# Kernel optimization log

Measured on AMD Instinct MI355X. Metric: run time of the kernel, lower is better.

Reference implementation:

```python
import jax, jax.numpy as jnp
import numpy as np

MARGIN = 0.2
EPS = 1e-8
N, D_EMB, N_CLASSES = 8192, 256, 512


def setup_inputs() -> dict:
    key = jax.random.key(0)
    k1, k2 = jax.random.split(key)
    embeddings = jax.random.normal(k1, (N, D_EMB), dtype=jnp.float32)
    labels = jax.random.randint(k2, (N,), 0, N_CLASSES, dtype=jnp.int64)
    return {"embeddings": embeddings, "labels": labels}


def reference(embeddings, labels):
    # OnlineTripleLoss.forward with sampling_strategy='fixed_semi_hard', cosine metric.
    n = embeddings.shape[0]
    norms = jnp.linalg.norm(embeddings, axis=1, keepdims=True)
    xn = embeddings / jnp.maximum(norms, EPS)
    dist = 1.0 - xn @ xn.T                       # [N, N] cosine distance

    same = labels[:, None] == labels[None, :]    # same-label mask
    neg_mask = ~same
    has_neg = jnp.any(neg_mask, axis=1)          # anchor has at least one negative

    # fixed_semi_hard argmax(ap+margin-an) == argmin(an); fallback is also argmin(an)
    BIG = jnp.float32(1e9)
    dmin_neg = jnp.min(jnp.where(neg_mask, dist, BIG), axis=1)  # [N]

    # all anchor-positive combinations: same label, a < p (itertools.combinations order)
    upper = jnp.triu(jnp.ones((n, n), dtype=bool), 1)
    pair_mask = same & upper & has_neg[:, None]

    losses = jnp.maximum(dist - dmin_neg[:, None] + MARGIN, 0.0)
    count = jnp.sum(pair_mask)
    loss_sum = jnp.sum(jnp.where(pair_mask, losses, 0.0))
    loss = jnp.where(count > 0, loss_sum / jnp.maximum(count, 1).astype(jnp.float32), 0.0)
    return loss, count
```

## Files before the change

kernel.cpp:

```cpp
#include <hip/hip_runtime.h>
#include <hip/hip_bf16.h>

#define NROWS 8192
#define DEMB 256
#define MARGIN 0.2f
#define BM 128
#define BK 64
#define NT (NROWS / BM)
#define NBLK (NT * (NT + 1) / 2)
#define NCLS 512
#define NCAP 96

typedef __attribute__((ext_vector_type(4))) float f32x4;
typedef __attribute__((ext_vector_type(8))) short bf16x8;

static __device__ __forceinline__ unsigned short f2b(float f) {
    unsigned u = __builtin_bit_cast(unsigned, f);
    u += 0x7fffu + ((u >> 16) & 1u);
    return (unsigned short)(u >> 16);
}
static __device__ __forceinline__ float b2f(unsigned short b) {
    unsigned u = ((unsigned)b) << 16;
    return __builtin_bit_cast(float, u);
}
static __device__ __forceinline__ unsigned encf(float f) {
    unsigned u = __builtin_bit_cast(unsigned, f);
    return (u & 0x80000000u) ? ~u : (u | 0x80000000u);
}
static __device__ __forceinline__ float decf(unsigned e) {
    unsigned u = (e & 0x80000000u) ? (e ^ 0x80000000u) : ~e;
    return __builtin_bit_cast(float, u);
}
static __device__ __forceinline__ void gload16(const void* g, void* l) {
    __builtin_amdgcn_global_load_lds(
        (const __attribute__((address_space(1))) unsigned int*)g,
        (__attribute__((address_space(3))) unsigned int*)l, 16, 0, 0);
}

__global__ __launch_bounds__(256) void k_norm(const float* __restrict__ x,
                                              unsigned short* __restrict__ xnb) {
    int row  = (blockIdx.x * blockDim.x + threadIdx.x) >> 6;
    int lane = threadIdx.x & 63;
    const float4* p = reinterpret_cast<const float4*>(x + (size_t)row * DEMB) + lane;
    float4 v = *p;
    float s = v.x * v.x + v.y * v.y + v.z * v.z + v.w * v.w;
#pragma unroll
    for (int m = 1; m < 64; m <<= 1) s += __shfl_xor(s, m);
    float inv = 1.0f / fmaxf(sqrtf(s), 1e-8f);
    ushort4 o;
    o.x = f2b(v.x * inv); o.y = f2b(v.y * inv);
    o.z = f2b(v.z * inv); o.w = f2b(v.w * inv);
    *(reinterpret_cast<ushort4*>(xnb + (size_t)row * DEMB) + lane) = o;
}

__global__ __launch_bounds__(256, 2) void k_maxneg(const unsigned short* __restrict__ xnb,
                                                   const int* __restrict__ labels,
                                                   unsigned* __restrict__ amax) {
    extern __shared__ char lds[];
    unsigned short* tile = (unsigned short*)lds;
    __shared__ int slabR[128], slabC[128];

    int tid  = threadIdx.x;
    int wid  = tid >> 6, lane = tid & 63;
    int wr   = wid >> 1, wc = wid & 1;
    int arow = lane & 15, kgrp = lane >> 4;
    int sw   = (arow & 7) << 4;

    int bi = 0, rem = blockIdx.x;
    while (rem >= NT - bi) { rem -= NT - bi; ++bi; }
    int bj = bi + rem;
    int i0 = bi * BM;
    int j0 = bj * BM;

    if (tid < 128)      slabR[tid]       = labels[i0 + tid];
    else                slabC[tid - 128] = labels[j0 + tid - 128];

    const unsigned short* Ag = xnb + (size_t)i0 * DEMB;
    const unsigned short* Bg = xnb + (size_t)j0 * DEMB;

    int c0 = (kgrp * 16) ^ sw;
    int c1 = (64 + kgrp * 16) ^ sw;
    int abase = (wr * 64 + arow) * 128;
    int bbase = (wc * 64 + arow) * 128;

    f32x4 acc[4][4] = {};

    auto stage = [&](int buf, int k0) {
#pragma unroll
        for (int i = 0; i < 4; ++i) {
            int idx  = i * 256 + tid;
            int row  = idx >> 3;
            int colb = (idx & 7) << 4;
            int scol = (colb ^ ((row & 7) << 4)) >> 1;
            const unsigned short* sa = Ag + (size_t)row * DEMB + k0 + scol;
            const unsigned short* sb = Bg + (size_t)row * DEMB + k0 + scol;
            unsigned short* da = tile + buf * 8192 + i * 2048 + wid * 512;
            unsigned short* db = tile + 16384 + buf * 8192 + i * 2048 + wid * 512;
            gload16(sa, da);
            gload16(sb, db);
        }
    };

    stage(0, 0);
#pragma unroll
    for (int ks = 0; ks < 4; ++ks) {
        __syncthreads();
        if (ks < 3) stage((ks + 1) & 1, (ks + 1) * BK);
        const char* At = (const char*)(tile + (ks & 1) * 8192);
        const char* Bt = (const char*)(tile + 16384 + (ks & 1) * 8192);
        bf16x8 a[4][2], b[4][2];
#pragma unroll
        for (int m = 0; m < 4; ++m) {
            a[m][0] = *(const bf16x8*)(At + abase + m * 2048 + c0);
            a[m][1] = *(const bf16x8*)(At + abase + m * 2048 + c1);
            b[m][0] = *(const bf16x8*)(Bt + bbase + m * 2048 + c0);
            b[m][1] = *(const bf16x8*)(Bt + bbase + m * 2048 + c1);
        }
#pragma unroll
        for (int m = 0; m < 4; ++m)
#pragma unroll
            for (int n = 0; n < 4; ++n) {
                acc[m][n] = __builtin_amdgcn_mfma_f32_16x16x32_bf16(a[m][0], b[n][0], acc[m][n], 0, 0, 0);
                acc[m][n] = __builtin_amdgcn_mfma_f32_16x16x32_bf16(a[m][1], b[n][1], acc[m][n], 0, 0, 0);
            }
    }

    __syncthreads();
    float* smaxr = (float*)tile;
    float* smaxc = (float*)tile + 256;

    int cl[4];
#pragma unroll
    for (int n = 0; n < 4; ++n) cl[n] = slabC[wc * 64 + n * 16 + arow];

    float cmx[4] = {-1e30f, -1e30f, -1e30f, -1e30f};
#pragma unroll
    for (int m = 0; m < 4; ++m) {
#pragma unroll
        for (int r = 0; r < 4; ++r) {
            int rl = slabR[wr * 64 + m * 16 + kgrp * 4 + r];
            float v = -1e30f;
#pragma unroll
            for (int n = 0; n < 4; ++n) {
                float av = acc[m][n][r];
                if (cl[n] != rl) {
                    v = fmaxf(v, av);
                    cmx[n] = fmaxf(cmx[n], av);
                }
            }
#pragma unroll
            for (int msk = 1; msk < 16; msk <<= 1) v = fmaxf(v, __shfl_xor(v, msk));
            if (arow == 0) smaxr[wc * 128 + wr * 64 + m * 16 + kgrp * 4 + r] = v;
        }
    }
#pragma unroll
    for (int n = 0; n < 4; ++n) {
        float w = cmx[n];
        w = fmaxf(w, __shfl_xor(w, 16));
        w = fmaxf(w, __shfl_xor(w, 32));
        if (kgrp == 0) smaxc[wr * 128 + wc * 64 + n * 16 + arow] = w;
    }
    __syncthreads();
    if (tid < 128) {
        float v = fmaxf(smaxr[tid], smaxr[128 + tid]);
        if (v > -1e29f) atomicMax(amax + i0 + tid, encf(v));
    } else {
        int t = tid - 128;
        float v = fmaxf(smaxc[t], smaxc[128 + t]);
        if (v > -1e29f) atomicMax(amax + j0 + t, encf(v));
    }
}

__global__ __launch_bounds__(256) void k_cpairs(const unsigned short* __restrict__ xnb,
                                                const int* __restrict__ labels,
                                                const unsigned* __restrict__ amax,
                                                float* __restrict__ closs,
                                                int* __restrict__ ccnt) {
    extern __shared__ char lds2[];
    int* slab = (int*)lds2;
    unsigned short* srows = (unsigned short*)lds2;
    __shared__ int clist[NCAP];
    __shared__ float sdm[NCAP];
    __shared__ unsigned char shn[NCAP];
    __shared__ unsigned short pl[NCAP * (NCAP - 1) / 2];
    __shared__ int wcnt[4], woff[4], snc;
    __shared__ float slloss[16];
    __shared__ int slcnt[16];

    int c   = blockIdx.x;
    int tid = threadIdx.x, wid = tid >> 6, lane = tid & 63;

    for (int i = tid; i < NROWS / 4; i += 256)
        ((int4*)slab)[i] = ((const int4*)labels)[i];
    __syncthreads();

    int base = wid * 2048;
    int cnt = 0;
    for (int s = 0; s < 8; ++s) {
        int b0 = base + s * 256;
        cnt += __popcll(__ballot(slab[b0 + lane] == c));
        cnt += __popcll(__ballot(slab[b0 + 64 + lane] == c));
        cnt += __popcll(__ballot(slab[b0 + 128 + lane] == c));
        cnt += __popcll(__ballot(slab[b0 + 192 + lane] == c));
    }
    if (lane == 0) wcnt[wid] = cnt;
    __syncthreads();
    if (tid == 0) {
        int o = 0;
        for (int w = 0; w < 4; ++w) { woff[w] = o; o += wcnt[w]; }
        snc = (o > NCAP) ? NCAP : o;
    }
    __syncthreads();
    int nc = snc;

    int off = woff[wid];
    for (int s = 0; s < 8; ++s) {
        int b0 = base + s * 256;
#pragma unroll
        for (int e = 0; e < 4; ++e) {
            int idx = b0 + e * 64 + lane;
            int l = slab[idx];
            unsigned long long m = __ballot(l == c);
            int rank = __popcll(m & ((1ull << lane) - 1ull));
            if (l == c && off + rank < NCAP) clist[off + rank] = idx;
            off += __popcll(m);
        }
    }
    __syncthreads();

    int nch = nc * 32;
    for (int ch = tid; ch < nch; ch += 256) {
        int r = ch >> 5, cc = ch & 31;
        *(bf16x8*)(srows + r * 256 + cc * 8) =
            *(const bf16x8*)(xnb + (size_t)clist[r] * DEMB + cc * 8);
    }
    if (tid < nc) {
        unsigned e = amax[clist[tid]];
        shn[tid] = (e != 0u);
        sdm[tid] = 1.0f - decf(e);
    }
    int npairs = nc * (nc - 1) / 2;
    for (int p = tid; p < npairs; p += 256) {
        int i = 0, rem = p;
        while (rem >= nc - 1 - i) { rem -= nc - 1 - i; ++i; }
        pl[p] = (unsigned short)((i << 8) | (i + 1 + rem));
    }
    __syncthreads();

    int slot = tid >> 4, gl = tid & 15;
    float gloss = 0.f;
    int gcnt = 0;
    for (int p = slot; p < npairs; p += 16) {
        int pr = pl[p], i = pr >> 8, j = pr & 255;
        bf16x8 a0 = *(const bf16x8*)(srows + i * 256 + gl * 16);
        bf16x8 a1 = *(const bf16x8*)(srows + i * 256 + gl * 16 + 8);
        bf16x8 b0 = *(const bf16x8*)(srows + j * 256 + gl * 16);
        bf16x8 b1 = *(const bf16x8*)(srows + j * 256 + gl * 16 + 8);
        float dot = 0.f;
#pragma unroll
        for (int e = 0; e < 8; ++e) {
            dot += b2f((unsigned short)a0[e]) * b2f((unsigned short)b0[e]);
            dot += b2f((unsigned short)a1[e]) * b2f((unsigned short)b1[e]);
        }
#pragma unroll
        for (int msk = 1; msk < 16; msk <<= 1) dot += __shfl_xor(dot, msk);
        if (gl == 0 && shn[i]) {
            gloss += fmaxf(1.0f - dot - sdm[i] + MARGIN, 0.0f);
            gcnt += 1;
        }
    }
    if (gl == 0) { slloss[slot] = gloss; slcnt[slot] = gcnt; }
    __syncthreads();
    if (tid == 0) {
        float s = 0.f; int k = 0;
        for (int q = 0; q < 16; ++q) { s += slloss[q]; k += slcnt[q]; }
        closs[c] = s; ccnt[c] = k;
    }
}

__global__ __launch_bounds__(256) void k_final(const float* __restrict__ closs,
                                               const int* __restrict__ ccnt,
                                               float* __restrict__ out) {
    __shared__ float sl[256];
    __shared__ int   sc[256];
    int tid = threadIdx.x;
    float s = closs[tid] + closs[tid + 256];
    int   k = ccnt[tid] + ccnt[tid + 256];
    sl[tid] = s; sc[tid] = k;
    __syncthreads();
    for (int st = 128; st > 0; st >>= 1) {
        if (tid < st) {
            sl[tid] += sl[tid + st];
            sc[tid] += sc[tid + st];
        }
        __syncthreads();
    }
    if (tid == 0) {
        out[0] = (sc[0] > 0) ? sl[0] / (float)sc[0] : 0.0f;
        out[1] = (float)sc[0];
    }
}

extern "C" void kernel_launch(void* const* d_in, const int* in_sizes, int n_in,
                              void* d_out, int out_size, void* d_ws, size_t ws_size,
                              hipStream_t stream) {
    const float* emb  = (const float*)d_in[0];
    const int* labels = (const int*)d_in[1];
    float* out = (float*)d_out;

    char* ws = (char*)d_ws;
    unsigned short* xnb = (unsigned short*)ws;
    unsigned* amax = (unsigned*)(ws + (size_t)4 * 1024 * 1024);
    float* closs   = (float*)   (ws + (size_t)4 * 1024 * 1024 + 32768);
    int*   ccnt    = (int*)     (ws + (size_t)4 * 1024 * 1024 + 40960);

    k_norm<<<NROWS / 4, 256, 0, stream>>>(emb, xnb);
    hipMemsetAsync(amax, 0, NROWS * sizeof(unsigned), stream);
    k_maxneg<<<NBLK, 256, 65536, stream>>>(xnb, labels, amax);
    k_cpairs<<<NCLS, 256, 49152, stream>>>(xnb, labels, amax, closs, ccnt);
    k_final<<<1, 256, 0, stream>>>(closs, ccnt, out);
}
```

Before: 88.29 us.

## Restructure max-negative GEMM to full grid with register-resident A rows

Replaces the triangular 128x128 tile grid with a full 64x8 grid where each 512-thread block keeps its 128 A rows in registers and streams eight B tiles through double-buffered LDS, keeping only per-row max reductions. This drops symmetric column maxima and the per-tile K-loop setup, at the cost of about twice the MFMA work and more register pressure. It also folds the amax memset into the norm kernel and makes k_cpairs read labels directly from global memory instead of staging them in LDS.

```diff
diff --git a/kernel.cpp b/kernel.cpp
--- a/kernel.cpp
+++ b/kernel.cpp
@@ -4,12 +4,10 @@
 #define NROWS 8192
 #define DEMB 256
 #define MARGIN 0.2f
-#define BM 128
-#define BK 64
-#define NT (NROWS / BM)
-#define NBLK (NT * (NT + 1) / 2)
 #define NCLS 512
 #define NCAP 96
+#define TPC 8
+#define NSTEP 16
 
 typedef __attribute__((ext_vector_type(4))) float f32x4;
 typedef __attribute__((ext_vector_type(8))) short bf16x8;
@@ -38,8 +36,11 @@
 }
 
 __global__ __launch_bounds__(256) void k_norm(const float* __restrict__ x,
-                                              unsigned short* __restrict__ xnb) {
-    int row  = (blockIdx.x * blockDim.x + threadIdx.x) >> 6;
+                                              unsigned short* __restrict__ xnb,
+                                              unsigned* __restrict__ amax) {
+    int gid = blockIdx.x * blockDim.x + threadIdx.x;
+    if (gid < NROWS) amax[gid] = 0u;
+    int row  = gid >> 6;
     int lane = threadIdx.x & 63;
     const float4* p = reinterpret_cast<const float4*>(x + (size_t)row * DEMB) + lane;
     float4 v = *p;
@@ -53,121 +54,120 @@
     *(reinterpret_cast<ushort4*>(xnb + (size_t)row * DEMB) + lane) = o;
 }
 
-__global__ __launch_bounds__(256, 2) void k_maxneg(const unsigned short* __restrict__ xnb,
+__global__ __launch_bounds__(512, 2) void k_maxneg(const unsigned short* __restrict__ xnb,
                                                    const int* __restrict__ labels,
                                                    unsigned* __restrict__ amax) {
     extern __shared__ char lds[];
-    unsigned short* tile = (unsigned short*)lds;
-    __shared__ int slabR[128], slabC[128];
+    unsigned short* Bl = (unsigned short*)lds;
 
     int tid  = threadIdx.x;
     int wid  = tid >> 6, lane = tid & 63;
     int wr   = wid >> 1, wc = wid & 1;
     int arow = lane & 15, kgrp = lane >> 4;
-    int sw   = (arow & 7) << 4;
-
-    int bi = 0, rem = blockIdx.x;
-    while (rem >= NT - bi) { rem -= NT - bi; ++bi; }
-    int bj = bi + rem;
-    int i0 = bi * BM;
-    int j0 = bj * BM;
-
-    if (tid < 128)      slabR[tid]       = labels[i0 + tid];
-    else                slabC[tid - 128] = labels[j0 + tid - 128];
-
-    const unsigned short* Ag = xnb + (size_t)i0 * DEMB;
-    const unsigned short* Bg = xnb + (size_t)j0 * DEMB;
-
-    int c0 = (kgrp * 16) ^ sw;
-    int c1 = (64 + kgrp * 16) ^ sw;
-    int abase = (wr * 64 + arow) * 128;
-    int bbase = (wc * 64 + arow) * 128;
-
-    f32x4 acc[4][4] = {};
-
-    auto stage = [&](int buf, int k0) {
-#pragma unroll
-        for (int i = 0; i < 4; ++i) {
-            int idx  = i * 256 + tid;
-            int row  = idx >> 3;
-            int colb = (idx & 7) << 4;
-            int scol = (colb ^ ((row & 7) << 4)) >> 1;
-            const unsigned short* sa = Ag + (size_t)row * DEMB + k0 + scol;
-            const unsigned short* sb = Bg + (size_t)row * DEMB + k0 + scol;
-            unsigned short* da = tile + buf * 8192 + i * 2048 + wid * 512;
-            unsigned short* db = tile + 16384 + buf * 8192 + i * 2048 + wid * 512;
-            gload16(sa, da);
-            gload16(sb, db);
+
+    int i0 = blockIdx.x * 128;
+    int j0 = blockIdx.y * (TPC * 128);
+
+    bf16x8 a[2][8];
+    const unsigned short* ap0 = xnb + (size_t)(i0 + wr * 32 + arow) * DEMB + kgrp * 8;
+#pragma unroll
+    for (int m = 0; m < 2; ++m)
+#pragma unroll
+        for (int kk = 0; kk < 8; ++kk)
+            a[m][kk] = *(const bf16x8*)(ap0 + m * 16 * DEMB + kk * 32);
+
+    int rlab[2][4];
+#pragma unroll
+    for (int m = 0; m < 2; ++m)
+#pragma unroll
+        for (int r = 0; r < 4; ++r)
+            rlab[m][r] = labels[i0 + wr * 32 + m * 16 + kgrp * 4 + r];
+
+    float rmax[2][4] = {{-1e30f, -1e30f, -1e30f, -1e30f},
+                        {-1e30f, -1e30f, -1e30f, -1e30f}};
+    f32x4 acc[2][4] = {};
+
+    auto stage = [&](int buf, int t, int h) {
+#pragma unroll
+        for (int is = 0; is < 4; ++is) {
+            int idx  = is * 512 + tid;
+            int row  = idx >> 4;
+            int colb = (idx & 15) << 4;
+            int scol = (colb ^ ((row & 15) << 4)) >> 1;
+            const unsigned short* src =
+                xnb + (size_t)(j0 + t * 128 + row) * DEMB + h * 128 + scol;
+            unsigned short* dst = Bl + buf * 16384 + is * 4096 + wid * 512;
+            gload16(src, dst);
         }
     };
 
-    stage(0, 0);
-#pragma unroll
-    for (int ks = 0; ks < 4; ++ks) {
+    int clab[4], nlab[4];
+    stage(0, 0, 0);
+#pragma unroll
+    for (int n = 0; n < 4; ++n) clab[n] = labels[j0 + wc * 64 + n * 16 + arow];
+
+    int sw = arow << 4;
+    for (int s = 0; s < NSTEP; ++s) {
         __syncthreads();
-        if (ks < 3) stage((ks + 1) & 1, (ks + 1) * BK);
-        const char* At = (const char*)(tile + (ks & 1) * 8192);
-        const char* Bt = (const char*)(tile + 16384 + (ks & 1) * 8192);
-        bf16x8 a[4][2], b[4][2];
-#pragma unroll
-        for (int m = 0; m < 4; ++m) {
-            a[m][0] = *(const bf16x8*)(At + abase + m * 2048 + c0);
-            a[m][1] = *(const bf16x8*)(At + abase + m * 2048 + c1);
-            b[m][0] = *(const bf16x8*)(Bt + bbase + m * 2048 + c0);
-            b[m][1] = *(const bf16x8*)(Bt + bbase + m * 2048 + c1);
-        }
-#pragma unroll
-        for (int m = 0; m < 4; ++m)
-#pragma unroll
-            for (int n = 0; n < 4; ++n) {
-                acc[m][n] = __builtin_amdgcn_mfma_f32_16x16x32_bf16(a[m][0], b[n][0], acc[m][n], 0, 0, 0);
-                acc[m][n] = __builtin_amdgcn_mfma_f32_16x16x32_bf16(a[m][1], b[n][1], acc[m][n], 0, 0, 0);
-            }
-    }
-
-    __syncthreads();
-    float* smaxr = (float*)tile;
-    float* smaxc = (float*)tile + 256;
-
-    int cl[4];
-#pragma unroll
-    for (int n = 0; n < 4; ++n) cl[n] = slabC[wc * 64 + n * 16 + arow];
-
-    float cmx[4] = {-1e30f, -1e30f, -1e30f, -1e30f};
-#pragma unroll
-    for (int m = 0; m < 4; ++m) {
+        if (s + 1 < NSTEP) stage((s + 1) & 1, (s + 1) >> 1, (s + 1) & 1);
+        int tile = s >> 1, h = s & 1;
+        if (h == 0 && tile + 1 < TPC) {
+#pragma unroll
+            for (int n = 0; n < 4; ++n)
+                nlab[n] = labels[j0 + (tile + 1) * 128 + wc * 64 + n * 16 + arow];
+        }
+        const char* Bt = (const char*)(Bl + (s & 1) * 16384);
+        bf16x8 b[4][4];
+#pragma unroll
+        for (int n = 0; n < 4; ++n) {
+            int rb = (wc * 64 + n * 16 + arow) * 256;
+#pragma unroll
+            for (int ksl = 0; ksl < 4; ++ksl)
+                b[n][ksl] = *(const bf16x8*)(Bt + rb + ((ksl * 64 + kgrp * 16) ^ sw));
+        }
+#pragma unroll
+        for (int m = 0; m < 2; ++m)
+#pragma unroll
+            for (int n = 0; n < 4; ++n)
+#pragma unroll
+                for (int ksl = 0; ksl < 4; ++ksl)
+                    acc[m][n] = __builtin_amdgcn_mfma_f32_16x16x32_bf16(
+                        a[m][h * 4 + ksl], b[n][ksl], acc[m][n], 0, 0, 0);
+        if (h == 1) {
+#pragma unroll
+            for (int m = 0; m < 2; ++m)
+#pragma unroll
+                for (int r = 0; r < 4; ++r) {
+                    float v = rmax[m][r];
+                    int rl = rlab[m][r];
+#pragma unroll
+                    for (int n = 0; n < 4; ++n)
+                        if (clab[n] != rl) v = fmaxf(v, acc[m][n][r]);
+                    rmax[m][r] = v;
+                }
+#pragma unroll
+            for (int m = 0; m < 2; ++m)
+#pragma unroll
+                for (int n = 0; n < 4; ++n) acc[m][n] = (f32x4){0.f, 0.f, 0.f, 0.f};
+#pragma unroll
+            for (int n = 0; n < 4; ++n) clab[n] = nlab[n];
+        }
+    }
+
+    float* smax = (float*)Bl;
+#pragma unroll
+    for (int m = 0; m < 2; ++m)
 #pragma unroll
         for (int r = 0; r < 4; ++r) {
-            int rl = slabR[wr * 64 + m * 16 + kgrp * 4 + r];
-            float v = -1e30f;
-#pragma unroll
-            for (int n = 0; n < 4; ++n) {
-                float av = acc[m][n][r];
-                if (cl[n] != rl) {
-                    v = fmaxf(v, av);
-                    cmx[n] = fmaxf(cmx[n], av);
-                }
-            }
+            float v = rmax[m][r];
 #pragma unroll
             for (int msk = 1; msk < 16; msk <<= 1) v = fmaxf(v, __shfl_xor(v, msk));
-            if (arow == 0) smaxr[wc * 128 + wr * 64 + m * 16 + kgrp * 4 + r] = v;
-        }
-    }
-#pragma unroll
-    for (int n = 0; n < 4; ++n) {
-        float w = cmx[n];
-        w = fmaxf(w, __shfl_xor(w, 16));
-        w = fmaxf(w, __shfl_xor(w, 32));
-        if (kgrp == 0) smaxc[wr * 128 + wc * 64 + n * 16 + arow] = w;
-    }
+            if (arow == 0) smax[wc * 128 + wr * 32 + m * 16 + kgrp * 4 + r] = v;
+        }
     __syncthreads();
     if (tid < 128) {
-        float v = fmaxf(smaxr[tid], smaxr[128 + tid]);
+        float v = fmaxf(smax[tid], smax[128 + tid]);
         if (v > -1e29f) atomicMax(amax + i0 + tid, encf(v));
-    } else {
-        int t = tid - 128;
-        float v = fmaxf(smaxc[t], smaxc[128 + t]);
-        if (v > -1e29f) atomicMax(amax + j0 + t, encf(v));
     }
 }
 
@@ -177,7 +177,6 @@
                                                 float* __restrict__ closs,
                                                 int* __restrict__ ccnt) {
     extern __shared__ char lds2[];
-    int* slab = (int*)lds2;
     unsigned short* srows = (unsigned short*)lds2;
     __shared__ int clist[NCAP];
     __shared__ float sdm[NCAP];
@@ -190,18 +189,13 @@
     int c   = blockIdx.x;
     int tid = threadIdx.x, wid = tid >> 6, lane = tid & 63;
 
-    for (int i = tid; i < NROWS / 4; i += 256)
-        ((int4*)slab)[i] = ((const int4*)labels)[i];
-    __syncthreads();
-
     int base = wid * 2048;
     int cnt = 0;
     for (int s = 0; s < 8; ++s) {
         int b0 = base + s * 256;
-        cnt += __popcll(__ballot(slab[b0 + lane] == c));
-        cnt += __popcll(__ballot(slab[b0 + 64 + lane] == c));
-        cnt += __popcll(__ballot(slab[b0 + 128 + lane] == c));
-        cnt += __popcll(__ballot(slab[b0 + 192 + lane] == c));
+#pragma unroll
+        for (int e = 0; e < 4; ++e)
+            cnt += __popcll(__ballot(labels[b0 + e * 64 + lane] == c));
     }
     if (lane == 0) wcnt[wid] = cnt;
     __syncthreads();
@@ -219,10 +213,10 @@
 #pragma unroll
         for (int e = 0; e < 4; ++e) {
             int idx = b0 + e * 64 + lane;
-            int l = slab[idx];
-            unsigned long long m = __ballot(l == c);
+            bool hit = (labels[idx] == c);
+            unsigned long long m = __ballot(hit);
             int rank = __popcll(m & ((1ull << lane) - 1ull));
-            if (l == c && off + rank < NCAP) clist[off + rank] = idx;
+            if (hit && off + rank < NCAP) clist[off + rank] = idx;
             off += __popcll(m);
         }
     }
@@ -314,9 +308,9 @@
     float* closs   = (float*)   (ws + (size_t)4 * 1024 * 1024 + 32768);
     int*   ccnt    = (int*)     (ws + (size_t)4 * 1024 * 1024 + 40960);
 
-    k_norm<<<NROWS / 4, 256, 0, stream>>>(emb, xnb);
-    hipMemsetAsync(amax, 0, NROWS * sizeof(unsigned), stream);
-    k_maxneg<<<NBLK, 256, 65536, stream>>>(xnb, labels, amax);
+    k_norm<<<NROWS / 4, 256, 0, stream>>>(emb, xnb, amax);
+    dim3 g2(NROWS / 128, NCLS / 64);
+    k_maxneg<<<g2, 512, 65536, stream>>>(xnb, labels, amax);
     k_cpairs<<<NCLS, 256, 49152, stream>>>(xnb, labels, amax, closs, ccnt);
     k_final<<<1, 256, 0, stream>>>(closs, ccnt, out);
 }
```

Measured after the change: 81.77 us. 7.4% less time.
